# Kernel tuning notes

Measured on AMD Instinct MI355X. Metric: run time of the kernel, lower is better.

Reference implementation:

```python
import jax, jax.numpy as jnp
import numpy as np

# --- static configuration (matches init_kwargs) ---
D = 20          # number of risky assets
N_NETS = 10     # number of policy sub-networks (after the initial linear one)
NN = 100        # number of SDE timesteps
DIFF = NN // N_NETS
H = 64          # hidden width of policy MLPs
B = 16384       # Monte-Carlo batch size
H_STEP = 0.01   # h = T / NN
R = 0.02        # risk-free rate (model.r)
MU = 0.06       # P-measure drift (model)
SIGMA = 0.2     # volatility
T_FIN = 1.0     # model.T
CURTAGE = 0.005
BN_EPS = 1e-3   # keras BatchNormalization epsilon


def _subnet(idx, x, uW_in, uW_h, ub_h, bn_g, bn_b, uW_out, ub_out):
    """SubNetwork forward (inference-mode BN: moving_mean=0, moving_var=1)."""
    inv = 1.0 / jnp.sqrt(1.0 + BN_EPS)
    Wi, Wh = uW_in[idx], uW_h[idx]
    b, g, bb = ub_h[idx], bn_g[idx], bn_b[idx]
    h = jax.nn.relu(x @ Wi + b[0]) * (inv * g[0]) + bb[0]
    h = jax.nn.relu(h @ Wh[0] + b[1]) * (inv * g[1]) + bb[1]
    h = jax.nn.relu(h @ Wh[1] + b[2]) * (inv * g[2]) + bb[2]
    return h @ uW_out[idx] + ub_out[idx]


def setup_inputs() -> dict:
    key = jax.random.key(0)
    ks = jax.random.split(key, 8)
    f = jnp.float32
    s = 0.1
    return {
        "x_in": 1.0 + 0.1 * jax.random.normal(ks[7], (B, 1), f),   # initial wealth ~1
        "S0": jnp.ones((B, D), f),                                  # initial (normalized) prices
        "dW": jax.random.normal(ks[0], (NN, B, D), f),              # standard normals, scaled by sqrt(h) inside
        "u0_W": jax.random.normal(ks[1], (1, D), f) * s,
        "u0_b": jnp.zeros((D,), f),
        "uW_in": jax.random.normal(ks[2], (N_NETS, 1, H), f) * s,
        "uW_h": jax.random.normal(ks[3], (N_NETS, 2, H, H), f) * (1.0 / np.sqrt(H)),
        "ub_h": jnp.zeros((N_NETS, 3, H), f),
        "bn_g": jnp.ones((N_NETS, 3, H), f),
        "bn_b": jnp.zeros((N_NETS, 3, H), f),
        "uW_out": jax.random.normal(ks[4], (N_NETS, H, D), f) * (1.0 / np.sqrt(H)),
        "ub_out": jnp.zeros((N_NETS, D), f),
        "opt_W": jax.random.normal(ks[5], (1, 2 * D + 1), f) * s,
        "opt_b": jnp.zeros((2 * D + 1,), f),
        "K_W": jax.random.normal(ks[6], (1, 2 * D), f) * s,
        "K_b": jnp.zeros((2 * D,), f),
    }


def reference(x_in, S0, dW, u0_W, u0_b, uW_in, uW_h, ub_h, bn_g, bn_b,
              uW_out, ub_out, opt_W, opt_b, K_W, K_b):
    # option allocation and strike heads (static linear SubNetworks)
    K_options = jax.nn.softmax(x_in @ opt_W + opt_b)[:, :2 * D]        # [B, 2D]
    alpha_tot = jnp.mean(jnp.sum(K_options, axis=1))                   # scalar
    K = 1.0 + 0.25 * jnp.tanh(x_in @ K_W + K_b)                        # [B, 2D]
    rescale = 1.0 - alpha_tot
    alpha0 = x_in @ u0_W + u0_b                                        # initial allocation [B, D]

    sqrt_h = jnp.sqrt(jnp.asarray(H_STEP, x_in.dtype))

    def step(carry, inp):
        x, S, S_Q, N_m1, dacc, alpha = carry
        n, dWn = inp
        u = alpha                                                      # amounts in risky assets [B, D]
        N_p = u / S                                                    # number of shares
        dacc = dacc + jnp.where(n > 1, jnp.abs(N_p - N_m1), 0.0)       # turnover accumulation
        dw = sqrt_h * dWn
        # self-financing wealth Euler step (model.F_x)
        x = (x + (x - jnp.sum(u, 1, keepdims=True)) * (R * H_STEP)
             + jnp.sum(u * (MU * H_STEP + SIGMA * dw), 1, keepdims=True))
        # log-Euler GBM steps under P (model.F_S) and Q (model_2.F_S)
        S = S * jnp.exp((MU - 0.5 * SIGMA ** 2) * H_STEP + SIGMA * dw)
        S_Q = S_Q * jnp.exp((R - 0.5 * SIGMA ** 2) * H_STEP + SIGMA * dw)
        # periodic policy update: network_u[n/diff](x) when n % diff == 0 and n < NN
        idx = jnp.clip(n // DIFF, 1, N_NETS) - 1
        new_alpha = _subnet(idx, x, uW_in, uW_h, ub_h, bn_g, bn_b, uW_out, ub_out)
        upd = (n % DIFF == 0) & (n < NN)
        alpha = jnp.where(upd, new_alpha, alpha)
        return (x, S, S_Q, N_p, dacc, alpha), None

    ns = jnp.arange(1, NN + 1)
    zeros_bd = jnp.zeros((B, D), x_in.dtype)
    init = (x_in, S0, jnp.ones((B, D), x_in.dtype), zeros_bd, zeros_bd, alpha0)
    (x, S, S_Q, _, dacc, _), _ = jax.lax.scan(step, init, (ns, dW))

    dacc_sum = jnp.sum(dacc, axis=1).reshape(x.shape)                  # [B, 1]
    disc = jnp.exp(jnp.asarray(-R * T_FIN, x.dtype))
    C0 = disc * jnp.mean(jnp.maximum(S_Q - K[:, :D], 0.0), axis=0)     # [D] MC call price
    P0 = disc * jnp.mean(jnp.maximum(K[:, D:] - S_Q, 0.0), axis=0)     # [D] MC put price
    C_T = jnp.maximum(S - K[:, :D], 0.0) / C0                          # [B, D]
    P_T = jnp.maximum(K[:, D:] - S, 0.0) / P0                          # [B, D]
    payoff = (jnp.sum(K_options[:, :D] * C_T, 1, keepdims=True)
              + jnp.sum(K_options[:, D:] * P_T, 1, keepdims=True))
    x = rescale * x - CURTAGE * rescale * dacc_sum + payoff            # options_in_p=True branch

    p5 = jnp.percentile(x, 5.0)
    p95 = jnp.percentile(x, 95.0)
    m_lo = x < p5
    m_hi = x > p95
    loss1 = -jnp.mean(x)
    loss2 = jnp.var(x)
    loss3 = -jnp.sum(jnp.where(m_lo, x, 0.0)) / jnp.maximum(jnp.sum(m_lo), 1)
    loss4 = -jnp.sum(jnp.where(m_hi, x, 0.0)) / jnp.maximum(jnp.sum(m_hi), 1)
    loss5 = jnp.mean(C_T[:, 0])
    loss6 = K[0, 1]
    loss7 = jnp.asarray(rescale)
    return tuple(jnp.reshape(l, (1,)) for l in
                 (loss1, loss2, loss3, loss4, loss5, loss6, loss7))
```

## Files before the change

### kernel.cpp

```cpp
#include <hip/hip_runtime.h>
#include <cstdint>
#include <cstddef>

#define B_TOT 16384
#define NSTEP 100

#define SQRT_H 0.1f
#define RH     2.0e-4f
#define MUH    6.0e-4f
#define DRIFT  4.0e-4f
#define SIGC   0.2f
#define SSC    0.02f
#define INVBN  0.99950037468877324f
#define QF     0.96078943915232318f
#define DISC   0.98019867330675525f
#define CURT   0.005f

typedef __attribute__((ext_vector_type(8))) short short8;
typedef __attribute__((ext_vector_type(4))) float floatx4;
typedef __attribute__((ext_vector_type(4))) unsigned uintx4;
typedef __attribute__((ext_vector_type(2))) unsigned uintx2;

__device__ __forceinline__ unsigned toSort(float f){
    unsigned u = __float_as_uint(f);
    return (u & 0x80000000u) ? ~u : (u | 0x80000000u);
}
__device__ __forceinline__ float fromSort(unsigned s){
    unsigned u = (s & 0x80000000u) ? (s & 0x7fffffffu) : ~s;
    return __uint_as_float(u);
}
__device__ __forceinline__ unsigned short bfc(float f){
    unsigned u = __float_as_uint(f);
    unsigned r = u + 0x7FFFu + ((u >> 16) & 1u);
    return (unsigned short)(r >> 16);
}
__device__ __forceinline__ float red16(float v){
    float t;
    t = __int_as_float(__builtin_amdgcn_update_dpp(0, __float_as_int(v), 0x128, 0xF, 0xF, false)); v += t;
    t = __int_as_float(__builtin_amdgcn_update_dpp(0, __float_as_int(v), 0x124, 0xF, 0xF, false)); v += t;
    t = __int_as_float(__builtin_amdgcn_update_dpp(0, __float_as_int(v), 0x122, 0xF, 0xF, false)); v += t;
    t = __int_as_float(__builtin_amdgcn_update_dpp(0, __float_as_int(v), 0x121, 0xF, 0xF, false)); v += t;
    return v;
}
__device__ __forceinline__ float tanh_fast(float z){
    z = fminf(9.f, fmaxf(-9.f, z));
    float e = __expf(2.f * z);
    return __fdividef(e - 1.f, e + 1.f);
}
__device__ __forceinline__ unsigned laneid(){
    return __builtin_amdgcn_mbcnt_hi(~0u, __builtin_amdgcn_mbcnt_lo(~0u, 0u));
}
__device__ __forceinline__ void aggAdd(unsigned* hist, unsigned bin){
    bool pending = true;
    unsigned lid = laneid();
    while (__any(pending)){
        if (pending){
            unsigned lead = (unsigned)__builtin_amdgcn_readfirstlane((int)bin);
            if (bin == lead){
                unsigned long long m = __ballot(1);
                if (lid == (unsigned)__builtin_ctzll(m))
                    atomicAdd(&hist[lead], (unsigned)__popcll(m));
                pending = false;
            }
        }
    }
}
__device__ __forceinline__ unsigned wexscan(unsigned s, int l){
    unsigned incl = s;
#pragma unroll
    for (int off=1; off<64; off<<=1){
        unsigned t2 = __shfl_up(incl, off, 64);
        if (l >= off) incl += t2;
    }
    return incl - s;
}

__global__ __launch_bounds__(256,1) void k_conv(
    const float* __restrict__ uWh, const float* __restrict__ ubh,
    const float* __restrict__ bng, const float* __restrict__ bnb,
    const float* __restrict__ uWout, const float* __restrict__ ubout,
    unsigned short* __restrict__ Wc2, unsigned short* __restrict__ Wc3,
    unsigned short* __restrict__ Wco,
    float* __restrict__ b2f, float* __restrict__ b3f, float* __restrict__ bof)
{
    const int p = blockIdx.x;
    const int t = threadIdx.x;
    __shared__ float g0s[64], g1s[64], g2s[64], e0s[64], e1s[64], e2s[64];
    __shared__ float red4[64][4];
    __shared__ float red8[32][8];
    if (t < 64){
        g0s[t] = INVBN * bng[(p*3+0)*64 + t]; e0s[t] = bnb[(p*3+0)*64 + t];
        g1s[t] = INVBN * bng[(p*3+1)*64 + t]; e1s[t] = bnb[(p*3+1)*64 + t];
        g2s[t] = INVBN * bng[(p*3+2)*64 + t]; e2s[t] = bnb[(p*3+2)*64 + t];
    }
    __syncthreads();
    {
        const int j = t & 63, kq = t >> 6;
        float bs = 0.f;
        for (int k = kq*16; k < kq*16+16; ++k){
            float w = uWh[((size_t)(p*2+0)*64 + k)*64 + j];
            bs += w * e0s[k];
            Wc2[(size_t)(p*64 + j)*64 + k] = bfc(w * g0s[k]);
        }
        red4[j][kq] = bs;
    }
    __syncthreads();
    if (t < 64) b2f[p*64 + t] = ubh[(p*3+1)*64 + t]
                 + red4[t][0]+red4[t][1]+red4[t][2]+red4[t][3];
    __syncthreads();
    {
        const int j = t & 63, kq = t >> 6;
        float bs = 0.f;
        for (int k = kq*16; k < kq*16+16; ++k){
            float w = uWh[((size_t)(p*2+1)*64 + k)*64 + j];
            bs += w * e1s[k];
            Wc3[(size_t)(p*64 + j)*64 + k] = bfc(w * g1s[k]);
        }
        red4[j][kq] = bs;
    }
    __syncthreads();
    if (t < 64) b3f[p*64 + t] = ubh[(p*3+2)*64 + t]
                 + red4[t][0]+red4[t][1]+red4[t][2]+red4[t][3];
    __syncthreads();
    {
        const int d = t & 31, kq = t >> 5;
        float bs = 0.f;
        for (int k = kq*8; k < kq*8+8; ++k){
            float w = (d < 20) ? uWout[((size_t)p*64 + k)*20 + d] : 0.f;
            bs += w * e2s[k];
            Wco[(size_t)(p*32 + d)*64 + k] = bfc(w * g2s[k]);
        }
        red8[d][kq] = bs;
    }
    __syncthreads();
    if (t < 32){
        float s = 0.f;
        for (int q=0;q<8;q++) s += red8[t][q];
        bof[p*32 + t] = ((t < 20) ? ubout[p*20 + t] : 0.f) + s;
    }
}

__global__ __launch_bounds__(256, 4) void k_sim(
    const float* __restrict__ x_in, const float* __restrict__ S0,
    const float* __restrict__ dW,
    const float* __restrict__ u0W, const float* __restrict__ u0b,
    const float* __restrict__ uWin, const float* __restrict__ ubh,
    const unsigned short* __restrict__ Wc2, const unsigned short* __restrict__ Wc3,
    const unsigned short* __restrict__ Wco,
    const float* __restrict__ b2f, const float* __restrict__ b3f,
    const float* __restrict__ bof,
    const float* __restrict__ optW, const float* __restrict__ optb,
    const float* __restrict__ KW, const float* __restrict__ Kb,
    float* __restrict__ xsim, float* __restrict__ daccs,
    float* __restrict__ Sfin, float* __restrict__ partial)
{
    __shared__ unsigned short hA[16*72];
    __shared__ unsigned short hB[16*72];
    __shared__ unsigned short WtA[64*72];
    __shared__ unsigned short WtB[64*72];
    __shared__ unsigned short WtO[32*72];
    __shared__ float aL[16*20];
    __shared__ float xL[16];
    __shared__ float pacc[48];

    const int tid = threadIdx.x;
    const int rl  = tid >> 4;
    const int la  = tid & 15;
    const int b   = blockIdx.x * 16 + rl;
    const int a2  = 16 + (la & 3);
    const bool act2 = (la < 4);
    const int w2 = tid >> 6;
    const int lw = tid & 63;
    const int cn = lw & 15;
    const int qq = lw >> 4;

    float x = x_in[b];
    const float S00 = S0[b*20 + la];
    const float S01 = S0[b*20 + a2];
    float iS0 = __fdividef(1.f, S00);
    float iS1 = __fdividef(1.f, S01);
    float al0 = fmaf(x, u0W[la], u0b[la]);
    float al1 = act2 ? fmaf(x, u0W[a2], u0b[a2]) : 0.f;
    float Nm10 = al0 * iS0, Nm11 = al1 * iS1;
    float dacc0 = 0.f, dacc1 = 0.f;

    const size_t STEP = (size_t)B_TOT * 20;
    const float* pA = dW + (size_t)b*20 + la;
    const float* pB = dW + (size_t)b*20 + a2;

    float dA[10], dB[10];
#pragma unroll
    for (int s = 0; s < 10; ++s){
        dA[s] = pA[(size_t)s*STEP];
        dB[s] = pB[(size_t)s*STEP];
    }
    const float XA = 1.f + RH;

    for (int p = 0; p < 10; ++p){
        const float su = red16(al0 + al1);
        const float Cp = su * (MUH - RH);
#pragma unroll
        for (int s = 0; s < 10; ++s){
            float np0 = al0 * iS0;
            float np1 = al1 * iS1;
            dacc0 += fabsf(np0 - Nm10);
            dacc1 += fabsf(np1 - Nm11);
            Nm10 = np0; Nm11 = np1;
            float dot = red16(fmaf(al0, dA[s], al1 * dB[s]));
            x = fmaf(SSC, dot, fmaf(x, XA, Cp));
            iS0 *= __expf(fmaf(-SSC, dA[s], -DRIFT));
            iS1 *= __expf(fmaf(-SSC, dB[s], -DRIFT));
        }
        if (p < 9){
            {
                const float* qA = pA + (size_t)(p+1)*10*STEP;
                const float* qB = pB + (size_t)(p+1)*10*STEP;
#pragma unroll
                for (int s = 0; s < 10; ++s){
                    dA[s] = qA[(size_t)s*STEP];
                    dB[s] = qB[(size_t)s*STEP];
                }
            }
            if (la == 0) xL[rl] = x;
            __syncthreads();
            {
                const unsigned short* W2p = Wc2 + (size_t)p*4096;
                const unsigned short* W3p = Wc3 + (size_t)p*4096;
                const int wr = tid >> 2, sg = (tid & 3) * 16;
                uintx4 v2a = *reinterpret_cast<const uintx4*>(W2p + wr*64 + sg);
                uintx4 v2b = *reinterpret_cast<const uintx4*>(W2p + wr*64 + sg + 8);
                uintx4 v3a = *reinterpret_cast<const uintx4*>(W3p + wr*64 + sg);
                uintx4 v3b = *reinterpret_cast<const uintx4*>(W3p + wr*64 + sg + 8);
                *reinterpret_cast<uintx4*>(&WtA[wr*72 + sg    ]) = v2a;
                *reinterpret_cast<uintx4*>(&WtA[wr*72 + sg + 8]) = v2b;
                *reinterpret_cast<uintx4*>(&WtB[wr*72 + sg    ]) = v3a;
                *reinterpret_cast<uintx4*>(&WtB[wr*72 + sg + 8]) = v3b;
                if (tid < 128){
                    const unsigned short* Wop = Wco + (size_t)p*2048;
                    uintx4 voa = *reinterpret_cast<const uintx4*>(Wop + wr*64 + sg);
                    uintx4 vob = *reinterpret_cast<const uintx4*>(Wop + wr*64 + sg + 8);
                    *reinterpret_cast<uintx4*>(&WtO[wr*72 + sg    ]) = voa;
                    *reinterpret_cast<uintx4*>(&WtO[wr*72 + sg + 8]) = vob;
                }
                const float xr = xL[tid & 15];
                const int u0 = (tid >> 4) * 4;
                const float* Wi = uWin + p*64;
                const float* b0 = ubh + (p*3+0)*64;
                unsigned short h4[4];
#pragma unroll
                for (int i=0;i<4;i++)
                    h4[i] = bfc(fmaxf(fmaf(xr, Wi[u0+i], b0[u0+i]), 0.f));
                uintx2 hw;
                hw.x = (unsigned)h4[0] | ((unsigned)h4[1] << 16);
                hw.y = (unsigned)h4[2] | ((unsigned)h4[3] << 16);
                *reinterpret_cast<uintx2*>(&hA[(tid&15)*72 + u0]) = hw;
            }
            __syncthreads();
            {
                const int col = 16*w2 + cn;
                float bias = b2f[p*64 + col];
                floatx4 c = {bias, bias, bias, bias};
                short8 a0 = *reinterpret_cast<const short8*>(&hA[cn*72 + qq*8]);
                short8 a1 = *reinterpret_cast<const short8*>(&hA[cn*72 + 32 + qq*8]);
                short8 bb0 = *reinterpret_cast<const short8*>(&WtA[col*72 + qq*8]);
                short8 bb1 = *reinterpret_cast<const short8*>(&WtA[col*72 + 32 + qq*8]);
                c = __builtin_amdgcn_mfma_f32_16x16x32_bf16(a0, bb0, c, 0, 0, 0);
                c = __builtin_amdgcn_mfma_f32_16x16x32_bf16(a1, bb1, c, 0, 0, 0);
#pragma unroll
                for (int i=0;i<4;i++)
                    hB[(qq*4+i)*72 + col] = bfc(fmaxf(c[i], 0.f));
            }
            __syncthreads();
            {
                const int col = 16*w2 + cn;
                float bias = b3f[p*64 + col];
                floatx4 c = {bias, bias, bias, bias};
                short8 a0 = *reinterpret_cast<const short8*>(&hB[cn*72 + qq*8]);
                short8 a1 = *reinterpret_cast<const short8*>(&hB[cn*72 + 32 + qq*8]);
                short8 bb0 = *reinterpret_cast<const short8*>(&WtB[col*72 + qq*8]);
                short8 bb1 = *reinterpret_cast<const short8*>(&WtB[col*72 + 32 + qq*8]);
                c = __builtin_amdgcn_mfma_f32_16x16x32_bf16(a0, bb0, c, 0, 0, 0);
                c = __builtin_amdgcn_mfma_f32_16x16x32_bf16(a1, bb1, c, 0, 0, 0);
#pragma unroll
                for (int i=0;i<4;i++)
                    hA[(qq*4+i)*72 + col] = bfc(fmaxf(c[i], 0.f));
            }
            __syncthreads();
            if (w2 < 2){
                const int col = 16*w2 + cn;
                float bias = bof[p*32 + col];
                floatx4 c = {bias, bias, bias, bias};
                short8 a0 = *reinterpret_cast<const short8*>(&hA[cn*72 + qq*8]);
                short8 a1 = *reinterpret_cast<const short8*>(&hA[cn*72 + 32 + qq*8]);
                short8 bb0 = *reinterpret_cast<const short8*>(&WtO[col*72 + qq*8]);
                short8 bb1 = *reinterpret_cast<const short8*>(&WtO[col*72 + 32 + qq*8]);
                c = __builtin_amdgcn_mfma_f32_16x16x32_bf16(a0, bb0, c, 0, 0, 0);
                c = __builtin_amdgcn_mfma_f32_16x16x32_bf16(a1, bb1, c, 0, 0, 0);
                if (col < 20){
#pragma unroll
                    for (int i=0;i<4;i++) aL[(qq*4+i)*20 + col] = c[i];
                }
            }
            __syncthreads();
            al0 = aL[rl*20 + la];
            al1 = act2 ? aL[rl*20 + a2] : 0.f;
        }
    }

    float Sf0 = __fdividef(1.f, iS0);
    float Sf1 = __fdividef(1.f, iS1);
    float ds = red16(dacc0 + dacc1);
    if (la == 0){ xsim[b] = x; daccs[b] = ds; }
    Sfin[b*20 + la] = Sf0;
    if (act2) Sfin[b*20 + a2] = Sf1;

    if (tid < 48) pacc[tid] = 0.f;
    __syncthreads();
    float e1v = __expf(fmaf(x, optW[la],    optb[la]));
    float e2v = __expf(fmaf(x, optW[16+la], optb[16+la]));
    float e3v = (la <= 8) ? __expf(fmaf(x, optW[32+la], optb[32+la])) : 0.f;
    float sAll = red16(e1v + e2v + e3v);
    float e40 = __shfl(e3v, (lw & 48) + 8, 64);
    float afrac = __fdividef(sAll - e40, sAll);
    float kc0 = fmaf(0.25f, tanh_fast(fmaf(x, KW[la],    Kb[la]   )), 1.f);
    float kp0 = fmaf(0.25f, tanh_fast(fmaf(x, KW[20+la], Kb[20+la])), 1.f);
    float sq0 = QF * __fdividef(Sf0, S00);
    atomicAdd(&pacc[la],    fmaxf(sq0 - kc0, 0.f));
    atomicAdd(&pacc[20+la], fmaxf(kp0 - sq0, 0.f));
    if (act2){
        float kc1 = fmaf(0.25f, tanh_fast(fmaf(x, KW[a2],    Kb[a2]   )), 1.f);
        float kp1 = fmaf(0.25f, tanh_fast(fmaf(x, KW[20+a2], Kb[20+a2])), 1.f);
        float sq1 = QF * __fdividef(Sf1, S01);
        atomicAdd(&pacc[a2],    fmaxf(sq1 - kc1, 0.f));
        atomicAdd(&pacc[20+a2], fmaxf(kp1 - sq1, 0.f));
    }
    if (la == 0){
        atomicAdd(&pacc[40], afrac);
        atomicAdd(&pacc[41], fmaxf(Sf0 - kc0, 0.f));
    }
    __syncthreads();
    if (tid < 48) partial[tid*1024 + blockIdx.x] = pacc[tid];
}

__global__ __launch_bounds__(256,1) void k_final(
    const float* __restrict__ x_in,
    const float* __restrict__ optW, const float* __restrict__ optb,
    const float* __restrict__ KW, const float* __restrict__ Kb,
    const float* __restrict__ Sfin, const float* __restrict__ xsim,
    const float* __restrict__ daccs, const float* __restrict__ partial,
    float* __restrict__ xfin, float* __restrict__ out)
{
    __shared__ float accL[48];
    __shared__ float tmp[48][4];
    const int t = threadIdx.x;
    if (t < 192){
        const int r = t >> 2, q = t & 3;
        const floatx4* s4 = (const floatx4*)(partial + r*1024 + q*256);
        float acc = 0.f;
#pragma unroll 4
        for (int i=0;i<64;i++){ floatx4 v = s4[i]; acc += v[0]+v[1]+v[2]+v[3]; }
        tmp[r][q] = acc;
    }
    __syncthreads();
    if (t < 48) accL[t] = tmp[t][0]+tmp[t][1]+tmp[t][2]+tmp[t][3];
    __syncthreads();

    const int b = blockIdx.x*256 + t;
    const float x = x_in[b];
    float e[41]; float m = -1e30f;
#pragma unroll
    for (int k=0;k<41;k++){ e[k] = fmaf(x, optW[k], optb[k]); m = fmaxf(m, e[k]); }
    float s = 0.f;
#pragma unroll
    for (int k=0;k<41;k++){ e[k] = __expf(e[k]-m); s += e[k]; }
    const float invs = 1.f / s;
    const float invB = 1.f / (float)B_TOT;
    const float rescale = 1.f - accL[40]*invB;
    float pay = 0.f, k01 = 0.f;
#pragma unroll
    for (int d=0; d<20; d++){
        float Sv = Sfin[(size_t)b*20 + d];
        float kc = fmaf(0.25f, tanh_fast(fmaf(x, KW[d],    Kb[d]   )), 1.f);
        float kp = fmaf(0.25f, tanh_fast(fmaf(x, KW[20+d], Kb[20+d])), 1.f);
        float C0d = DISC * accL[d]    * invB;
        float P0d = DISC * accL[20+d] * invB;
        pay += (e[d]*invs)    * fmaxf(Sv - kc, 0.f) / C0d;
        pay += (e[20+d]*invs) * fmaxf(kp - Sv, 0.f) / P0d;
        if (d == 1) k01 = kc;
    }
    float xf = rescale * xsim[b] - CURT * rescale * daccs[b] + pay;
    xfin[b] = xf;
    if (b == 0){
        out[4] = accL[41] / (DISC * accL[0]);
        out[5] = k01;
        out[6] = rescale;
    }
}

__global__ __launch_bounds__(1024,1) void k_tail(
    const float* __restrict__ xfin, float* __restrict__ out)
{
    __shared__ unsigned keys[16384];
    __shared__ unsigned hist[4096];
    __shared__ unsigned b1[4], r1[4], b2[4], r2[4];
    __shared__ int rep1[4], rep2[4];
    __shared__ float vals[4];
    __shared__ float pp[2];
    __shared__ double rdd[16][2];
    __shared__ float rff[16][2];
    __shared__ unsigned ruu[16][2];
    const int tid = threadIdx.x;
    const unsigned ranks[4] = {819u, 820u, 15563u, 15564u};

#pragma unroll
    for (int i=0;i<16;i++) keys[tid + i*1024] = toSort(xfin[tid + i*1024]);
#pragma unroll
    for (int i=0;i<4;i++) hist[tid + i*1024] = 0u;
    __syncthreads();

#pragma unroll
    for (int i=0;i<16;i++) aggAdd(hist, keys[tid + i*1024] >> 20);
    __syncthreads();
    if (tid < 64){
        const int l = tid;
        unsigned s = 0;
#pragma unroll
        for (int i=0;i<16;i++){
            const int j = (i + l) & 15;
            uintx4 v = *reinterpret_cast<const uintx4*>(&hist[l*64 + j*4]);
            s += v.x + v.y + v.z + v.w;
        }
        const unsigned cumb = wexscan(s, l);
#pragma unroll
        for (int t=0;t<4;t++){
            const unsigned r = ranks[t];
            bool own = (r >= cumb) && (r < cumb + s);
            unsigned long long m = __ballot(own);
            int owner = (int)__builtin_ctzll(m);
            unsigned cb = (unsigned)__shfl((int)cumb, owner, 64);
            unsigned rr = r - cb;
            unsigned c = hist[owner*64 + l];
            unsigned cex = wexscan(c, l);
            if (rr >= cex && rr < cex + c){
                b1[t] = (unsigned)(owner*64 + l);
                r1[t] = rr - cex;
            }
        }
    }
    __syncthreads();
    if (tid == 0){
#pragma unroll
        for (int t=0;t<4;t++)
            rep1[t] = (t>0 && b1[t]==b1[t-1]) ? rep1[t-1] : t;
    }
    __syncthreads();

#pragma unroll
    for (int i=0;i<4;i++) hist[tid + i*1024] = 0u;
    __syncthreads();
#pragma unroll
    for (int i=0;i<16;i++){
        unsigned k = keys[tid + i*1024];
        unsigned h12 = k >> 20, mid = (k >> 10) & 1023u;
#pragma unroll
        for (int t=0;t<4;t++)
            if (rep1[t]==t && h12 == b1[t]) atomicAdd(&hist[t*1024 + (int)mid], 1u);
    }
    __syncthreads();
    if (tid < 256){
        const int p = tid >> 6, l = tid & 63;
        const unsigned* h = hist + rep1[p]*1024;
        unsigned s = 0;
#pragma unroll
        for (int i=0;i<4;i++){
            const int j = (i + l) & 3;
            uintx4 v = *reinterpret_cast<const uintx4*>(&h[l*16 + j*4]);
            s += v.x + v.y + v.z + v.w;
        }
        const unsigned cumb = wexscan(s, l);
        const unsigned r = r1[p];
        bool own = (r >= cumb) && (r < cumb + s);
        unsigned long long m = __ballot(own);
        int owner = (int)__builtin_ctzll(m);
        unsigned cb = (unsigned)__shfl((int)cumb, owner, 64);
        unsigned rr = r - cb;
        unsigned c = (l < 16) ? h[owner*16 + l] : 0u;
        unsigned cex = wexscan(c, l);
        if (l < 16 && rr >= cex && rr < cex + c){
            b2[p] = (unsigned)(owner*16 + l);
            r2[p] = rr - cex;
        }
    }
    __syncthreads();
    if (tid == 0){
#pragma unroll
        for (int t=0;t<4;t++)
            rep2[t] = (t>0 && b1[t]==b1[t-1] && b2[t]==b2[t-1]) ? rep2[t-1] : t;
    }
    __syncthreads();

#pragma unroll
    for (int i=0;i<4;i++) hist[tid + i*1024] = 0u;
    __syncthreads();
#pragma unroll
    for (int i=0;i<16;i++){
        unsigned k = keys[tid + i*1024];
        unsigned top22 = k >> 10;
#pragma unroll
        for (int t=0;t<4;t++)
            if (rep2[t]==t && top22 == ((b1[t]<<10) | b2[t]))
                atomicAdd(&hist[t*1024 + (int)(k & 1023u)], 1u);
    }
    __syncthreads();
    if (tid < 256){
        const int p = tid >> 6, l = tid & 63;
        const unsigned* h = hist + rep2[p]*1024;
        unsigned s = 0;
#pragma unroll
        for (int i=0;i<4;i++){
            const int j = (i + l) & 3;
            uintx4 v = *reinterpret_cast<const uintx4*>(&h[l*16 + j*4]);
            s += v.x + v.y + v.z + v.w;
        }
        const unsigned cumb = wexscan(s, l);
        const unsigned r = r2[p];
        bool own = (r >= cumb) && (r < cumb + s);
        unsigned long long m = __ballot(own);
        int owner = (int)__builtin_ctzll(m);
        unsigned cb = (unsigned)__shfl((int)cumb, owner, 64);
        unsigned rr = r - cb;
        unsigned c = (l < 16) ? h[owner*16 + l] : 0u;
        unsigned cex = wexscan(c, l);
        if (l < 16 && rr >= cex && rr < cex + c){
            vals[p] = fromSort((b1[p]<<20) | (b2[p]<<10) | (unsigned)(owner*16 + l));
        }
    }
    __syncthreads();
    if (tid == 0){
        pp[0] = vals[0] + 0.15f*(vals[1]-vals[0]);
        pp[1] = vals[2] + 0.85f*(vals[3]-vals[2]);
    }
    __syncthreads();

    const float p5 = pp[0], p95 = pp[1];
    double sv = 0.0, sq = 0.0;
    float lo = 0.f, hi = 0.f;
    unsigned lc = 0u, hc = 0u;
#pragma unroll
    for (int i=0;i<16;i++){
        float v = fromSort(keys[tid + i*1024]);
        sv += (double)v; sq += (double)v*(double)v;
        if (v < p5){ lo += v; lc++; }
        if (v > p95){ hi += v; hc++; }
    }
    for (int o=1;o<64;o<<=1){
        sv += __shfl_xor(sv,o,64);
        sq += __shfl_xor(sq,o,64);
        lo += __shfl_xor(lo,o,64);
        hi += __shfl_xor(hi,o,64);
        lc += __shfl_xor(lc,o,64);
        hc += __shfl_xor(hc,o,64);
    }
    const int wv = tid >> 6, ln = tid & 63;
    if (ln == 0){ rdd[wv][0]=sv; rdd[wv][1]=sq; rff[wv][0]=lo; rff[wv][1]=hi;
                  ruu[wv][0]=lc; ruu[wv][1]=hc; }
    __syncthreads();
    if (tid == 0){
        double a=0, bq=0; float c=0, d=0; unsigned e2=0, f2=0;
        for (int i=0;i<16;i++){ a+=rdd[i][0]; bq+=rdd[i][1]; c+=rff[i][0];
                                 d+=rff[i][1]; e2+=ruu[i][0]; f2+=ruu[i][1]; }
        const double N = (double)B_TOT;
        double mean = a / N;
        out[0] = (float)(-mean);
        out[1] = (float)(bq/N - mean*mean);
        out[2] = -c / (float)(e2 ? e2 : 1u);
        out[3] = -d / (float)(f2 ? f2 : 1u);
    }
}

extern "C" void kernel_launch(void* const* d_in, const int* in_sizes, int n_in,
                              void* d_out, int out_size, void* d_ws, size_t ws_size,
                              hipStream_t stream)
{
    const float* x_in = (const float*)d_in[0];
    const float* S0   = (const float*)d_in[1];
    const float* dW   = (const float*)d_in[2];
    const float* u0W  = (const float*)d_in[3];
    const float* u0b  = (const float*)d_in[4];
    const float* uWin = (const float*)d_in[5];
    const float* uWh  = (const float*)d_in[6];
    const float* ubh  = (const float*)d_in[7];
    const float* bng  = (const float*)d_in[8];
    const float* bnb  = (const float*)d_in[9];
    const float* uWout= (const float*)d_in[10];
    const float* ubout= (const float*)d_in[11];
    const float* optW = (const float*)d_in[12];
    const float* optb = (const float*)d_in[13];
    const float* KW   = (const float*)d_in[14];
    const float* Kb   = (const float*)d_in[15];
    float* out = (float*)d_out;
    float* ws  = (float*)d_ws;

    const size_t OFF_XSIM = 0;
    const size_t OFF_DACC = 16384;
    const size_t OFF_S    = 32768;
    const size_t OFF_XFIN = 360448;
    const size_t OFF_PART = 376832;
    const size_t OFF_WC2  = 425984;
    const size_t OFF_WC3  = 446464;
    const size_t OFF_WCO  = 466944;
    const size_t OFF_B2F  = 477184;
    const size_t OFF_B3F  = 477824;
    const size_t OFF_BOF  = 478464;

    unsigned short* Wc2 = (unsigned short*)(ws + OFF_WC2);
    unsigned short* Wc3 = (unsigned short*)(ws + OFF_WC3);
    unsigned short* Wco = (unsigned short*)(ws + OFF_WCO);

    k_conv<<<10,256,0,stream>>>(uWh, ubh, bng, bnb, uWout, ubout,
                                Wc2, Wc3, Wco,
                                ws+OFF_B2F, ws+OFF_B3F, ws+OFF_BOF);
    k_sim<<<1024,256,0,stream>>>(x_in, S0, dW, u0W, u0b, uWin, ubh,
                                 Wc2, Wc3, Wco,
                                 ws+OFF_B2F, ws+OFF_B3F, ws+OFF_BOF,
                                 optW, optb, KW, Kb,
                                 ws+OFF_XSIM, ws+OFF_DACC, ws+OFF_S, ws+OFF_PART);
    k_final<<<64,256,0,stream>>>(x_in, optW, optb, KW, Kb,
                                 ws+OFF_S, ws+OFF_XSIM, ws+OFF_DACC, ws+OFF_PART,
                                 ws+OFF_XFIN, out);
    k_tail<<<1,1024,0,stream>>>(ws+OFF_XFIN, out);
}
```

Before: 304.2 us.

## Load MFMA weight fragments straight from global memory and split weight conversion across blocks

k_sim no longer stages the per-subnet weight matrices in shared memory. Each lane now loads its own bf16 B-fragments directly from global (L2-resident) memory into registers. This removes the LDS copy, the xL broadcast and one barrier per subnet, and shrinks shared memory use, which may allow more blocks per CU. The first-layer input is computed from the lane's own x, since the 16 lanes of a row share it. k_conv is split into 30 blocks (one per subnet and layer) to add parallelism, at the cost of more uncoalesced global loads in the hot loop.

```diff
diff --git a/kernel.cpp b/kernel.cpp
--- a/kernel.cpp
+++ b/kernel.cpp
@@ -83,60 +83,48 @@
     unsigned short* __restrict__ Wco,
     float* __restrict__ b2f, float* __restrict__ b3f, float* __restrict__ bof)
 {
-    const int p = blockIdx.x;
+    const int bid = blockIdx.x;
+    const int p = bid / 3, m = bid % 3;
     const int t = threadIdx.x;
-    __shared__ float g0s[64], g1s[64], g2s[64], e0s[64], e1s[64], e2s[64];
+    __shared__ float gs[64], es[64];
     __shared__ float red4[64][4];
     __shared__ float red8[32][8];
     if (t < 64){
-        g0s[t] = INVBN * bng[(p*3+0)*64 + t]; e0s[t] = bnb[(p*3+0)*64 + t];
-        g1s[t] = INVBN * bng[(p*3+1)*64 + t]; e1s[t] = bnb[(p*3+1)*64 + t];
-        g2s[t] = INVBN * bng[(p*3+2)*64 + t]; e2s[t] = bnb[(p*3+2)*64 + t];
-    }
-    __syncthreads();
-    {
+        gs[t] = INVBN * bng[(p*3+m)*64 + t];
+        es[t] = bnb[(p*3+m)*64 + t];
+    }
+    __syncthreads();
+    if (m < 2){
+        unsigned short* Wt = (m == 0) ? Wc2 : Wc3;
         const int j = t & 63, kq = t >> 6;
         float bs = 0.f;
         for (int k = kq*16; k < kq*16+16; ++k){
-            float w = uWh[((size_t)(p*2+0)*64 + k)*64 + j];
-            bs += w * e0s[k];
-            Wc2[(size_t)(p*64 + j)*64 + k] = bfc(w * g0s[k]);
+            float w = uWh[((size_t)(p*2+m)*64 + k)*64 + j];
+            bs += w * es[k];
+            Wt[(size_t)(p*64 + j)*64 + k] = bfc(w * gs[k]);
         }
         red4[j][kq] = bs;
-    }
-    __syncthreads();
-    if (t < 64) b2f[p*64 + t] = ubh[(p*3+1)*64 + t]
-                 + red4[t][0]+red4[t][1]+red4[t][2]+red4[t][3];
-    __syncthreads();
-    {
-        const int j = t & 63, kq = t >> 6;
-        float bs = 0.f;
-        for (int k = kq*16; k < kq*16+16; ++k){
-            float w = uWh[((size_t)(p*2+1)*64 + k)*64 + j];
-            bs += w * e1s[k];
-            Wc3[(size_t)(p*64 + j)*64 + k] = bfc(w * g1s[k]);
-        }
-        red4[j][kq] = bs;
-    }
-    __syncthreads();
-    if (t < 64) b3f[p*64 + t] = ubh[(p*3+2)*64 + t]
-                 + red4[t][0]+red4[t][1]+red4[t][2]+red4[t][3];
-    __syncthreads();
-    {
+        __syncthreads();
+        if (t < 64){
+            float v = ubh[(p*3+m+1)*64 + t]
+                    + red4[t][0]+red4[t][1]+red4[t][2]+red4[t][3];
+            if (m == 0) b2f[p*64 + t] = v; else b3f[p*64 + t] = v;
+        }
+    } else {
         const int d = t & 31, kq = t >> 5;
         float bs = 0.f;
         for (int k = kq*8; k < kq*8+8; ++k){
             float w = (d < 20) ? uWout[((size_t)p*64 + k)*20 + d] : 0.f;
-            bs += w * e2s[k];
-            Wco[(size_t)(p*32 + d)*64 + k] = bfc(w * g2s[k]);
+            bs += w * es[k];
+            Wco[(size_t)(p*32 + d)*64 + k] = bfc(w * gs[k]);
         }
         red8[d][kq] = bs;
-    }
-    __syncthreads();
-    if (t < 32){
-        float s = 0.f;
-        for (int q=0;q<8;q++) s += red8[t][q];
-        bof[p*32 + t] = ((t < 20) ? ubout[p*20 + t] : 0.f) + s;
+        __syncthreads();
+        if (t < 32){
+            float s = 0.f;
+            for (int q=0;q<8;q++) s += red8[t][q];
+            bof[p*32 + t] = ((t < 20) ? ubout[p*20 + t] : 0.f) + s;
+        }
     }
 }
 
@@ -156,11 +144,7 @@
 {
     __shared__ unsigned short hA[16*72];
     __shared__ unsigned short hB[16*72];
-    __shared__ unsigned short WtA[64*72];
-    __shared__ unsigned short WtB[64*72];
-    __shared__ unsigned short WtO[32*72];
     __shared__ float aL[16*20];
-    __shared__ float xL[16];
     __shared__ float pacc[48];
 
     const int tid = threadIdx.x;
@@ -221,81 +205,60 @@
                     dB[s] = qB[(size_t)s*STEP];
                 }
             }
-            if (la == 0) xL[rl] = x;
-            __syncthreads();
+            const int col = 16*w2 + cn;
+            const unsigned short* W2p = Wc2 + (size_t)p*4096 + (size_t)col*64;
+            const unsigned short* W3p = Wc3 + (size_t)p*4096 + (size_t)col*64;
+            short8 wA0 = *reinterpret_cast<const short8*>(W2p + qq*8);
+            short8 wA1 = *reinterpret_cast<const short8*>(W2p + 32 + qq*8);
+            short8 wB0 = *reinterpret_cast<const short8*>(W3p + qq*8);
+            short8 wB1 = *reinterpret_cast<const short8*>(W3p + 32 + qq*8);
             {
-                const unsigned short* W2p = Wc2 + (size_t)p*4096;
-                const unsigned short* W3p = Wc3 + (size_t)p*4096;
-                const int wr = tid >> 2, sg = (tid & 3) * 16;
-                uintx4 v2a = *reinterpret_cast<const uintx4*>(W2p + wr*64 + sg);
-                uintx4 v2b = *reinterpret_cast<const uintx4*>(W2p + wr*64 + sg + 8);
-                uintx4 v3a = *reinterpret_cast<const uintx4*>(W3p + wr*64 + sg);
-                uintx4 v3b = *reinterpret_cast<const uintx4*>(W3p + wr*64 + sg + 8);
-                *reinterpret_cast<uintx4*>(&WtA[wr*72 + sg    ]) = v2a;
-                *reinterpret_cast<uintx4*>(&WtA[wr*72 + sg + 8]) = v2b;
-                *reinterpret_cast<uintx4*>(&WtB[wr*72 + sg    ]) = v3a;
-                *reinterpret_cast<uintx4*>(&WtB[wr*72 + sg + 8]) = v3b;
-                if (tid < 128){
-                    const unsigned short* Wop = Wco + (size_t)p*2048;
-                    uintx4 voa = *reinterpret_cast<const uintx4*>(Wop + wr*64 + sg);
-                    uintx4 vob = *reinterpret_cast<const uintx4*>(Wop + wr*64 + sg + 8);
-                    *reinterpret_cast<uintx4*>(&WtO[wr*72 + sg    ]) = voa;
-                    *reinterpret_cast<uintx4*>(&WtO[wr*72 + sg + 8]) = vob;
-                }
-                const float xr = xL[tid & 15];
-                const int u0 = (tid >> 4) * 4;
                 const float* Wi = uWin + p*64;
                 const float* b0 = ubh + (p*3+0)*64;
                 unsigned short h4[4];
 #pragma unroll
                 for (int i=0;i<4;i++)
-                    h4[i] = bfc(fmaxf(fmaf(xr, Wi[u0+i], b0[u0+i]), 0.f));
+                    h4[i] = bfc(fmaxf(fmaf(x, Wi[la*4+i], b0[la*4+i]), 0.f));
                 uintx2 hw;
                 hw.x = (unsigned)h4[0] | ((unsigned)h4[1] << 16);
                 hw.y = (unsigned)h4[2] | ((unsigned)h4[3] << 16);
-                *reinterpret_cast<uintx2*>(&hA[(tid&15)*72 + u0]) = hw;
+                *reinterpret_cast<uintx2*>(&hA[rl*72 + la*4]) = hw;
             }
             __syncthreads();
             {
-                const int col = 16*w2 + cn;
                 float bias = b2f[p*64 + col];
                 floatx4 c = {bias, bias, bias, bias};
                 short8 a0 = *reinterpret_cast<const short8*>(&hA[cn*72 + qq*8]);
                 short8 a1 = *reinterpret_cast<const short8*>(&hA[cn*72 + 32 + qq*8]);
-                short8 bb0 = *reinterpret_cast<const short8*>(&WtA[col*72 + qq*8]);
-                short8 bb1 = *reinterpret_cast<const short8*>(&WtA[col*72 + 32 + qq*8]);
-                c = __builtin_amdgcn_mfma_f32_16x16x32_bf16(a0, bb0, c, 0, 0, 0);
-                c = __builtin_amdgcn_mfma_f32_16x16x32_bf16(a1, bb1, c, 0, 0, 0);
+                c = __builtin_amdgcn_mfma_f32_16x16x32_bf16(a0, wA0, c, 0, 0, 0);
+                c = __builtin_amdgcn_mfma_f32_16x16x32_bf16(a1, wA1, c, 0, 0, 0);
 #pragma unroll
                 for (int i=0;i<4;i++)
                     hB[(qq*4+i)*72 + col] = bfc(fmaxf(c[i], 0.f));
             }
             __syncthreads();
             {
-                const int col = 16*w2 + cn;
                 float bias = b3f[p*64 + col];
                 floatx4 c = {bias, bias, bias, bias};
                 short8 a0 = *reinterpret_cast<const short8*>(&hB[cn*72 + qq*8]);
                 short8 a1 = *reinterpret_cast<const short8*>(&hB[cn*72 + 32 + qq*8]);
-                short8 bb0 = *reinterpret_cast<const short8*>(&WtB[col*72 + qq*8]);
-                short8 bb1 = *reinterpret_cast<const short8*>(&WtB[col*72 + 32 + qq*8]);
-                c = __builtin_amdgcn_mfma_f32_16x16x32_bf16(a0, bb0, c, 0, 0, 0);
-                c = __builtin_amdgcn_mfma_f32_16x16x32_bf16(a1, bb1, c, 0, 0, 0);
+                c = __builtin_amdgcn_mfma_f32_16x16x32_bf16(a0, wB0, c, 0, 0, 0);
+                c = __builtin_amdgcn_mfma_f32_16x16x32_bf16(a1, wB1, c, 0, 0, 0);
 #pragma unroll
                 for (int i=0;i<4;i++)
                     hA[(qq*4+i)*72 + col] = bfc(fmaxf(c[i], 0.f));
             }
             __syncthreads();
             if (w2 < 2){
-                const int col = 16*w2 + cn;
+                const unsigned short* Wop = Wco + (size_t)p*2048 + (size_t)col*64;
+                short8 wO0 = *reinterpret_cast<const short8*>(Wop + qq*8);
+                short8 wO1 = *reinterpret_cast<const short8*>(Wop + 32 + qq*8);
                 float bias = bof[p*32 + col];
                 floatx4 c = {bias, bias, bias, bias};
                 short8 a0 = *reinterpret_cast<const short8*>(&hA[cn*72 + qq*8]);
                 short8 a1 = *reinterpret_cast<const short8*>(&hA[cn*72 + 32 + qq*8]);
-                short8 bb0 = *reinterpret_cast<const short8*>(&WtO[col*72 + qq*8]);
-                short8 bb1 = *reinterpret_cast<const short8*>(&WtO[col*72 + 32 + qq*8]);
-                c = __builtin_amdgcn_mfma_f32_16x16x32_bf16(a0, bb0, c, 0, 0, 0);
-                c = __builtin_amdgcn_mfma_f32_16x16x32_bf16(a1, bb1, c, 0, 0, 0);
+                c = __builtin_amdgcn_mfma_f32_16x16x32_bf16(a0, wO0, c, 0, 0, 0);
+                c = __builtin_amdgcn_mfma_f32_16x16x32_bf16(a1, wO1, c, 0, 0, 0);
                 if (col < 20){
 #pragma unroll
                     for (int i=0;i<4;i++) aL[(qq*4+i)*20 + col] = c[i];
@@ -617,7 +580,7 @@
     unsigned short* Wc3 = (unsigned short*)(ws + OFF_WC3);
     unsigned short* Wco = (unsigned short*)(ws + OFF_WCO);
 
-    k_conv<<<10,256,0,stream>>>(uWh, ubh, bng, bnb, uWout, ubout,
+    k_conv<<<30,256,0,stream>>>(uWh, ubh, bng, bnb, uWout, ubout,
                                 Wc2, Wc3, Wco,
                                 ws+OFF_B2F, ws+OFF_B3F, ws+OFF_BOF);
     k_sim<<<1024,256,0,stream>>>(x_in, S0, dW, u0W, u0b, uWin, ubh,
```

New measurement: 301.9 us. Within noise of the previous version (-0.8%).
